# Kernel tuning notes

Hardware: AMD Instinct MI355X
Metric: run time of the kernel (lower is better)

Reference implementation:

```python
import jax, jax.numpy as jnp
import numpy as np

N = 50000      # nodes
E = 800000     # edges (before self-loops)
IN = 128       # in_channels
HID = 64       # hidden_channels (= per-head dim, concat=False)
H = 4          # heads
OUT = 40       # out_channels
L = 4          # num_layers
LN_EPS = 1e-5


def setup_inputs() -> dict:
    key = jax.random.key(0)
    ks = jax.random.split(key, 12)
    s = 0.05
    return {
        "x": jax.random.normal(ks[0], (N, IN), jnp.float32),
        "edge_index": jax.random.randint(ks[1], (2, E), 0, N, dtype=jnp.int32),
        "Wi": jax.random.normal(ks[2], (IN, HID), jnp.float32) * s,
        "bi": jnp.zeros((HID,), jnp.float32),
        "lin_W": jax.random.normal(ks[3], (L, HID, H * HID), jnp.float32) * s,
        "att_src": jax.random.normal(ks[4], (L, H, HID), jnp.float32) * s,
        "att_dst": jax.random.normal(ks[5], (L, H, HID), jnp.float32) * s,
        "gat_b": jnp.zeros((L, HID), jnp.float32),
        "ln_g": jnp.ones((L, HID), jnp.float32),
        "ln_b": jnp.zeros((L, HID), jnp.float32),
        "Wo": jax.random.normal(ks[6], (HID, OUT), jnp.float32) * s,
        "bo": jnp.zeros((OUT,), jnp.float32),
    }


def _layer_norm(x, g, b):
    mu = jnp.mean(x, axis=-1, keepdims=True)
    var = jnp.mean(jnp.square(x - mu), axis=-1, keepdims=True)
    return (x - mu) * jax.lax.rsqrt(var + LN_EPS) * g + b


def _gat_conv(x, src, dst, W, a_src, a_dst, bias):
    # PyG GATConv: heads=H, out_channels=HID, concat=False (mean over heads),
    # negative_slope=0.2, self-loops already appended to (src, dst).
    xl = (x @ W).reshape(N, H, HID)                    # [N,H,C]
    alpha_s = jnp.einsum('nhc,hc->nh', xl, a_src)      # [N,H]
    alpha_d = jnp.einsum('nhc,hc->nh', xl, a_dst)      # [N,H]
    e = jax.nn.leaky_relu(alpha_s[src] + alpha_d[dst], 0.2)  # [Etot,H]
    # segment softmax over incoming edges of each destination node
    m = jax.ops.segment_max(e, dst, num_segments=N)    # [N,H]
    e = jnp.exp(e - m[dst])
    denom = jax.ops.segment_sum(e, dst, num_segments=N)
    alpha = e / (denom[dst] + 1e-16)                   # [Etot,H]
    msg = alpha[:, :, None] * xl[src]                  # [Etot,H,C]
    out = jax.ops.segment_sum(msg, dst, num_segments=N)  # [N,H,C]
    return out.mean(axis=1) + bias                     # concat=False -> mean


def reference(x, edge_index, Wi, bi, lin_W, att_src, att_dst, gat_b, ln_g, ln_b, Wo, bo):
    # add self-loops (GATConv default add_self_loops=True)
    loops = jnp.arange(N, dtype=edge_index.dtype)
    src = jnp.concatenate([edge_index[0], loops])
    dst = jnp.concatenate([edge_index[1], loops])

    h = jax.nn.elu(x @ Wi + bi)
    for i in range(L):
        residual = h
        h = _gat_conv(h, src, dst, lin_W[i], att_src[i], att_dst[i], gat_b[i])
        h = _layer_norm(h, ln_g[i], ln_b[i])
        h = jax.nn.elu(h)
        if i > 0:
            h = h + residual
        # dropout p=0.0 -> identity
    return h @ Wo + bo
```

## Files before the change

kernel.cpp:

```cpp
#include <hip/hip_runtime.h>
#include <hip/hip_bf16.h>

#define N_NODES 50000
#define N_EDGES 800000
#define E_TOT   (N_EDGES + N_NODES)
#define IN_CH   128
#define HID     64
#define HEADS   4
#define OUT_CH  40
#define LAYERS  4
#define LN_EPS  1e-5f

#define AG_STRIDE  262
#define WC_STRIDE  68

__device__ __forceinline__ unsigned short f2bf(float f) {
    unsigned u = __float_as_uint(f);
    unsigned r = (u + 0x7fffu + ((u >> 16) & 1u)) >> 16;
    return (unsigned short)r;
}
__device__ __forceinline__ float bf_lo(unsigned u) { return __uint_as_float(u << 16); }
__device__ __forceinline__ float bf_hi(unsigned u) { return __uint_as_float(u & 0xffff0000u); }
__device__ __forceinline__ float lrelu(float x) { return x > 0.f ? x : 0.2f * x; }

__device__ __forceinline__ unsigned fenc(float f) {
    unsigned u = __float_as_uint(f);
    return (u & 0x80000000u) ? ~u : (u | 0x80000000u);
}
__device__ __forceinline__ float fdec(unsigned k) {
    unsigned u = (k & 0x80000000u) ? (k & 0x7fffffffu) : ~k;
    return __uint_as_float(u);
}


__global__ void k_hist(const int* __restrict__ ei, int* __restrict__ cnt,
                       int* __restrict__ rank) {
    int e = blockIdx.x * blockDim.x + threadIdx.x;
    if (e >= E_TOT) return;
    int dst = (e < N_EDGES) ? ei[N_EDGES + e] : (e - N_EDGES);
    rank[e] = atomicAdd(&cnt[dst], 1);
}

__global__ __launch_bounds__(1024) void k_scan_a(const int* __restrict__ cnt,
                                                 int* __restrict__ row_ptr,
                                                 int* __restrict__ bsum) {
    __shared__ int wt[16];
    int tid = threadIdx.x, lane = tid & 63, w = tid >> 6;
    int i = blockIdx.x * 1024 + tid;
    int v = (i < N_NODES) ? cnt[i] : 0;
    int x = v;
    for (int off = 1; off < 64; off <<= 1) {
        int t = __shfl_up(x, off, 64);
        if (lane >= off) x += t;
    }
    if (lane == 63) wt[w] = x;
    __syncthreads();
    if (w == 0) {
        int t = (lane < 16) ? wt[lane] : 0;
        for (int off = 1; off < 16; off <<= 1) {
            int u = __shfl_up(t, off, 64);
            if (lane >= off) t += u;
        }
        if (lane < 16) wt[lane] = t;
    }
    __syncthreads();
    int woff = (w > 0) ? wt[w - 1] : 0;
    if (i < N_NODES) row_ptr[i] = woff + x - v;
    if (tid == 0) bsum[blockIdx.x] = wt[15];
}

#define SCAN_BLOCKS 49

__global__ __launch_bounds__(64) void k_scan_b(const int* __restrict__ bsum,
                                               int* __restrict__ boff,
                                               int* __restrict__ row_ptr) {
    int lane = threadIdx.x;
    int v = (lane < SCAN_BLOCKS) ? bsum[lane] : 0;
    int x = v;
    for (int off = 1; off < 64; off <<= 1) {
        int t = __shfl_up(x, off, 64);
        if (lane >= off) x += t;
    }
    if (lane < SCAN_BLOCKS) boff[lane] = x - v;
    if (lane == 63) row_ptr[N_NODES] = x;
}

__global__ __launch_bounds__(256) void k_scan_c(int* __restrict__ row_ptr,
                                                const int* __restrict__ boff) {
    int i = blockIdx.x * 256 + threadIdx.x;
    if (i >= N_NODES) return;
    row_ptr[i] += boff[i >> 10];
}

__global__ void k_scatter(const int* __restrict__ ei,
                          const int* __restrict__ row_ptr,
                          const int* __restrict__ rank,
                          int* __restrict__ csr_src) {
    int e = blockIdx.x * blockDim.x + threadIdx.x;
    if (e >= E_TOT) return;
    int src, dst;
    if (e < N_EDGES) { src = ei[e]; dst = ei[N_EDGES + e]; }
    else             { src = dst = e - N_EDGES; }
    int pos = row_ptr[dst] + rank[e];
    csr_src[pos] = src;
}


__global__ __launch_bounds__(256) void k_prep(const float* __restrict__ lin_W,
                                              const float* __restrict__ att_src,
                                              const float* __restrict__ att_dst,
                                              float* __restrict__ watt,
                                              float* __restrict__ wstack) {
    int l = blockIdx.x, tid = threadIdx.x;
    const float* Wl = lin_W + (size_t)l * HID * 256;
    {
        int k = tid, h = k >> 6, i = k & 63;
        const float* src = Wl + i * 256 + h * 64;
        float* dstp = wstack + (size_t)l * 256 * 64 + k * 64;
        for (int c = 0; c < 64; c += 4)
            *(float4*)(dstp + c) = *(const float4*)(src + c);
    }
    for (int idx = tid; idx < 512; idx += 256) {
        int v = idx >> 6, i = idx & 63;
        int h = v & 3;
        const float* av = (v < 4 ? att_src : att_dst) + (size_t)l * 256 + h * 64;
        const float* wr = Wl + i * 256 + h * 64;
        float p = 0.f;
        for (int c = 0; c < 64; ++c) p = fmaf(wr[c], av[c], p);
        watt[(size_t)l * 512 + v * 64 + i] = p;
    }
}


__global__ __launch_bounds__(256) void k_gemm_in(const float* __restrict__ x,
                                                 const float* __restrict__ Wi,
                                                 const float* __restrict__ bi,
                                                 const float* __restrict__ watt,
                                                 float* __restrict__ h,
                                                 unsigned short* __restrict__ h_bf,
                                                 float* __restrict__ alpha_s,
                                                 float* __restrict__ alpha_d,
                                                 unsigned* __restrict__ mxk) {
    __shared__ float xT[IN_CH * 64];
    __shared__ float Ws[IN_CH * HID];
    __shared__ float wl[512];
    __shared__ unsigned s_mx[4];
    int tid = threadIdx.x;
    int row0 = blockIdx.x * 64;
    if (tid < 4) s_mx[tid] = 0;
    for (int i = tid; i < 512; i += 256) wl[i] = watt[i];
    for (int i = tid * 4; i < IN_CH * HID; i += 1024)
        *(float4*)(Ws + i) = *(const float4*)(Wi + i);
    {
        int r = tid >> 2, k0 = (tid & 3) * 32;
        int rr = row0 + r;
#pragma unroll
        for (int j = 0; j < 32; j += 4) {
            float4 v = (rr < N_NODES) ? *(const float4*)(x + (size_t)rr * IN_CH + k0 + j)
                                      : make_float4(0.f, 0.f, 0.f, 0.f);
            xT[(k0 + j    ) * 64 + r] = v.x;
            xT[(k0 + j + 1) * 64 + r] = v.y;
            xT[(k0 + j + 2) * 64 + r] = v.z;
            xT[(k0 + j + 3) * 64 + r] = v.w;
        }
    }
    __syncthreads();
    int tx = tid & 15, ty = tid >> 4;
    int c0 = tx * 4, r0 = ty * 4;
    float acc[4][4] = {};
    for (int k = 0; k < IN_CH; ++k) {
        float4 xv = *(const float4*)(xT + k * 64 + r0);
        float4 wv = *(const float4*)(Ws + k * HID + c0);
        float xr[4] = {xv.x, xv.y, xv.z, xv.w};
        float wc[4] = {wv.x, wv.y, wv.z, wv.w};
#pragma unroll
        for (int r = 0; r < 4; ++r)
#pragma unroll
            for (int c = 0; c < 4; ++c)
                acc[r][c] = fmaf(xr[r], wc[c], acc[r][c]);
    }
    float4 bv = *(const float4*)(bi + c0);
    float bcs[4] = {bv.x, bv.y, bv.z, bv.w};
    float rpmax[4] = {-1e30f, -1e30f, -1e30f, -1e30f};
#pragma unroll
    for (int r = 0; r < 4; ++r) {
        int rr = row0 + r0 + r;
        float vv[4];
#pragma unroll
        for (int c = 0; c < 4; ++c) {
            float t = acc[r][c] + bcs[c];
            vv[c] = t > 0.f ? t : (__expf(t) - 1.f);
        }
        if (rr < N_NODES) {
            *(float4*)(h + (size_t)rr * HID + c0) = make_float4(vv[0], vv[1], vv[2], vv[3]);
            unsigned short t4[4] = {f2bf(vv[0]), f2bf(vv[1]), f2bf(vv[2]), f2bf(vv[3])};
            *(uint2*)(h_bf + (size_t)rr * HID + c0) = *(uint2*)t4;
        }
        float red[8];
#pragma unroll
        for (int v = 0; v < 8; ++v) {
            const float* wv = wl + v * 64 + c0;
            float p = vv[0]*wv[0] + vv[1]*wv[1] + vv[2]*wv[2] + vv[3]*wv[3];
            p += __shfl_xor(p, 1, 64);
            p += __shfl_xor(p, 2, 64);
            p += __shfl_xor(p, 4, 64);
            p += __shfl_xor(p, 8, 64);
            red[v] = p;
        }
        if (tx == 0 && rr < N_NODES) {
            *(float4*)(alpha_s + (size_t)rr * 4) = make_float4(red[0], red[1], red[2], red[3]);
            *(float4*)(alpha_d + (size_t)rr * 4) = make_float4(red[4], red[5], red[6], red[7]);
#pragma unroll
            for (int hh = 0; hh < 4; ++hh) rpmax[hh] = fmaxf(rpmax[hh], red[hh]);
        }
    }
    if (tx == 0) {
#pragma unroll
        for (int hh = 0; hh < 4; ++hh) atomicMax(&s_mx[hh], fenc(rpmax[hh]));
    }
    __syncthreads();
    if (tid < 4) atomicMax(&mxk[tid], s_mx[tid]);
}


__global__ __launch_bounds__(256) void k_aggregate(
    const unsigned short* __restrict__ h_bf,
    const float* __restrict__ alpha_s,
    const float* __restrict__ alpha_d,
    const int* __restrict__ row_ptr,
    const int* __restrict__ csr_src,
    const unsigned* __restrict__ mxk,
    unsigned short* __restrict__ agg)
{
    int tid = threadIdx.x;
    int d = blockIdx.x * 32 + (tid >> 3);
    int q = tid & 7;
    if (d >= N_NODES) return;
    int start = row_ptr[d], end = row_ptr[d + 1];

    float4 ad = *(const float4*)(alpha_d + (size_t)d * 4);
    float mp0 = lrelu(fdec(mxk[0]) + ad.x);
    float mp1 = lrelu(fdec(mxk[1]) + ad.y);
    float mp2 = lrelu(fdec(mxk[2]) + ad.z);
    float mp3 = lrelu(fdec(mxk[3]) + ad.w);

    float acc[4][8] = {};
    float ds0 = 0.f, ds1 = 0.f, ds2 = 0.f, ds3 = 0.f;

    int s = csr_src[start];
    for (int e = start; e < end; ++e) {
        int sn = (e + 1 < end) ? csr_src[e + 1] : 0;
        float4 as = *(const float4*)(alpha_s + (size_t)s * 4);
        uint4 u = *(const uint4*)(h_bf + ((size_t)s << 6) + (q << 3));
        float w0 = __expf(lrelu(as.x + ad.x) - mp0);
        float w1 = __expf(lrelu(as.y + ad.y) - mp1);
        float w2 = __expf(lrelu(as.z + ad.z) - mp2);
        float w3 = __expf(lrelu(as.w + ad.w) - mp3);
        ds0 += w0; ds1 += w1; ds2 += w2; ds3 += w3;
        float f0 = bf_lo(u.x), f1 = bf_hi(u.x), f2 = bf_lo(u.y), f3 = bf_hi(u.y);
        float f4 = bf_lo(u.z), f5 = bf_hi(u.z), f6 = bf_lo(u.w), f7 = bf_hi(u.w);
        acc[0][0] = fmaf(w0, f0, acc[0][0]); acc[0][1] = fmaf(w0, f1, acc[0][1]);
        acc[0][2] = fmaf(w0, f2, acc[0][2]); acc[0][3] = fmaf(w0, f3, acc[0][3]);
        acc[0][4] = fmaf(w0, f4, acc[0][4]); acc[0][5] = fmaf(w0, f5, acc[0][5]);
        acc[0][6] = fmaf(w0, f6, acc[0][6]); acc[0][7] = fmaf(w0, f7, acc[0][7]);
        acc[1][0] = fmaf(w1, f0, acc[1][0]); acc[1][1] = fmaf(w1, f1, acc[1][1]);
        acc[1][2] = fmaf(w1, f2, acc[1][2]); acc[1][3] = fmaf(w1, f3, acc[1][3]);
        acc[1][4] = fmaf(w1, f4, acc[1][4]); acc[1][5] = fmaf(w1, f5, acc[1][5]);
        acc[1][6] = fmaf(w1, f6, acc[1][6]); acc[1][7] = fmaf(w1, f7, acc[1][7]);
        acc[2][0] = fmaf(w2, f0, acc[2][0]); acc[2][1] = fmaf(w2, f1, acc[2][1]);
        acc[2][2] = fmaf(w2, f2, acc[2][2]); acc[2][3] = fmaf(w2, f3, acc[2][3]);
        acc[2][4] = fmaf(w2, f4, acc[2][4]); acc[2][5] = fmaf(w2, f5, acc[2][5]);
        acc[2][6] = fmaf(w2, f6, acc[2][6]); acc[2][7] = fmaf(w2, f7, acc[2][7]);
        acc[3][0] = fmaf(w3, f0, acc[3][0]); acc[3][1] = fmaf(w3, f1, acc[3][1]);
        acc[3][2] = fmaf(w3, f2, acc[3][2]); acc[3][3] = fmaf(w3, f3, acc[3][3]);
        acc[3][4] = fmaf(w3, f4, acc[3][4]); acc[3][5] = fmaf(w3, f5, acc[3][5]);
        acc[3][6] = fmaf(w3, f6, acc[3][6]); acc[3][7] = fmaf(w3, f7, acc[3][7]);
        s = sn;
    }

    float inv[4] = {1.f / (ds0 + 1e-16f), 1.f / (ds1 + 1e-16f),
                    1.f / (ds2 + 1e-16f), 1.f / (ds3 + 1e-16f)};
    size_t base = (size_t)d * 256 + (q << 3);
#pragma unroll
    for (int hh = 0; hh < 4; ++hh) {
        unsigned short t8[8];
#pragma unroll
        for (int k = 0; k < 8; ++k) t8[k] = f2bf(acc[hh][k] * inv[hh]);
        *(uint4*)(agg + base + hh * 64) = *(uint4*)t8;
    }
}


__global__ __launch_bounds__(256) void k_post(const unsigned short* __restrict__ agg,
                                              const float* __restrict__ wstack,
                                              const float* __restrict__ gat_b,
                                              const float* __restrict__ ln_g,
                                              const float* __restrict__ ln_b,
                                              const float* __restrict__ h_res,
                                              const float* __restrict__ watt_next,
                                              float* __restrict__ h_out,
                                              unsigned short* __restrict__ hbf_out,
                                              float* __restrict__ alpha_s,
                                              float* __restrict__ alpha_d,
                                              unsigned* __restrict__ mxk_next,
                                              int use_res, int do_alpha) {
    __shared__ unsigned short aS[32 * AG_STRIDE];
    __shared__ float Wc[32 * WC_STRIDE];
    __shared__ unsigned s_mx[4];
    int tid = threadIdx.x;
    int row0 = blockIdx.x * 32;
    if (tid < 4) s_mx[tid] = 0;
    {
        int r = tid & 31, kc = (tid >> 5) * 32;
        int rr = row0 + r;
        unsigned short* dstp = aS + r * AG_STRIDE + kc;
        if (rr < N_NODES) {
            const unsigned short* src = agg + (size_t)rr * 256 + kc;
#pragma unroll
            for (int j = 0; j < 8; ++j)
                *(uint2*)(dstp + j * 4) = *(const uint2*)(src + j * 4);
        } else {
            uint2 z = make_uint2(0, 0);
#pragma unroll
            for (int j = 0; j < 8; ++j) *(uint2*)(dstp + j * 4) = z;
        }
    }

    int tx = tid & 15, ty = tid >> 4;
    int c0 = tx * 4, r0 = ty * 2;
    float acc[2][4] = {};

    int wk = tid >> 3;
    int wc8 = (tid & 7) * 8;
    for (int chunk = 0; chunk < 8; ++chunk) {
        __syncthreads();
        {
            const float* wsrc = wstack + (size_t)(chunk * 32 + wk) * 64 + wc8;
            float* wdst = Wc + wk * WC_STRIDE + wc8;
            *(float4*)(wdst)     = *(const float4*)(wsrc);
            *(float4*)(wdst + 4) = *(const float4*)(wsrc + 4);
        }
        __syncthreads();
        int kbase = chunk * 32;
#pragma unroll
        for (int kb = 0; kb < 8; ++kb) {
            int kl = kb * 4;
            float4 w0 = *(const float4*)(Wc + (kl + 0) * WC_STRIDE + c0);
            float4 w1 = *(const float4*)(Wc + (kl + 1) * WC_STRIDE + c0);
            float4 w2 = *(const float4*)(Wc + (kl + 2) * WC_STRIDE + c0);
            float4 w3 = *(const float4*)(Wc + (kl + 3) * WC_STRIDE + c0);
#pragma unroll
            for (int r = 0; r < 2; ++r) {
                uint2 au = *(const uint2*)(aS + (r0 + r) * AG_STRIDE + kbase + kl);
                float a0 = bf_lo(au.x), a1 = bf_hi(au.x), a2 = bf_lo(au.y), a3 = bf_hi(au.y);
                acc[r][0] = fmaf(a0, w0.x, fmaf(a1, w1.x, fmaf(a2, w2.x, fmaf(a3, w3.x, acc[r][0]))));
                acc[r][1] = fmaf(a0, w0.y, fmaf(a1, w1.y, fmaf(a2, w2.y, fmaf(a3, w3.y, acc[r][1]))));
                acc[r][2] = fmaf(a0, w0.z, fmaf(a1, w1.z, fmaf(a2, w2.z, fmaf(a3, w3.z, acc[r][2]))));
                acc[r][3] = fmaf(a0, w0.w, fmaf(a1, w1.w, fmaf(a2, w2.w, fmaf(a3, w3.w, acc[r][3]))));
            }
        }
    }

    float4 gb = *(const float4*)(gat_b + c0);
    float bias[4] = {gb.x, gb.y, gb.z, gb.w};
    float4 lg = *(const float4*)(ln_g + c0);
    float4 lb = *(const float4*)(ln_b + c0);
    float gg[4] = {lg.x, lg.y, lg.z, lg.w};
    float bb[4] = {lb.x, lb.y, lb.z, lb.w};
    float rpmax[4] = {-1e30f, -1e30f, -1e30f, -1e30f};
#pragma unroll
    for (int r = 0; r < 2; ++r) {
        int rr = row0 + r0 + r;
        float o[4];
#pragma unroll
        for (int c = 0; c < 4; ++c) o[c] = acc[r][c] * 0.25f + bias[c];
        float s = o[0] + o[1] + o[2] + o[3];
        float s2 = o[0]*o[0] + o[1]*o[1] + o[2]*o[2] + o[3]*o[3];
        for (int off = 1; off < 16; off <<= 1) {
            s  += __shfl_xor(s,  off, 64);
            s2 += __shfl_xor(s2, off, 64);
        }
        float mu = s * (1.f / 64.f);
        float var = s2 * (1.f / 64.f) - mu * mu;
        float rstd = rsqrtf(var + LN_EPS);
        float vv[4];
#pragma unroll
        for (int c = 0; c < 4; ++c) {
            float t = (o[c] - mu) * rstd * gg[c] + bb[c];
            vv[c] = t > 0.f ? t : (__expf(t) - 1.f);
        }
        if (rr < N_NODES) {
            if (use_res) {
                float4 rv = *(const float4*)(h_res + (size_t)rr * HID + c0);
                vv[0] += rv.x; vv[1] += rv.y; vv[2] += rv.z; vv[3] += rv.w;
            }
            *(float4*)(h_out + (size_t)rr * HID + c0) = make_float4(vv[0], vv[1], vv[2], vv[3]);
            unsigned short t4[4] = {f2bf(vv[0]), f2bf(vv[1]), f2bf(vv[2]), f2bf(vv[3])};
            *(uint2*)(hbf_out + (size_t)rr * HID + c0) = *(uint2*)t4;
        }
        if (do_alpha) {
            float red[8];
#pragma unroll
            for (int v = 0; v < 8; ++v) {
                const float* wv = watt_next + v * 64 + c0;
                float p = vv[0]*wv[0] + vv[1]*wv[1] + vv[2]*wv[2] + vv[3]*wv[3];
                p += __shfl_xor(p, 1, 64);
                p += __shfl_xor(p, 2, 64);
                p += __shfl_xor(p, 4, 64);
                p += __shfl_xor(p, 8, 64);
                red[v] = p;
            }
            if (tx == 0 && rr < N_NODES) {
                *(float4*)(alpha_s + (size_t)rr * 4) = make_float4(red[0], red[1], red[2], red[3]);
                *(float4*)(alpha_d + (size_t)rr * 4) = make_float4(red[4], red[5], red[6], red[7]);
#pragma unroll
                for (int hh = 0; hh < 4; ++hh) rpmax[hh] = fmaxf(rpmax[hh], red[hh]);
            }
        }
    }
    if (do_alpha) {
        if (tx == 0) {
#pragma unroll
            for (int hh = 0; hh < 4; ++hh) atomicMax(&s_mx[hh], fenc(rpmax[hh]));
        }
        __syncthreads();
        if (tid < 4) atomicMax(&mxk_next[tid], s_mx[tid]);
    }
}


__global__ __launch_bounds__(256) void k_gemm_out(const float* __restrict__ h,
                                                  const float* __restrict__ Wo,
                                                  const float* __restrict__ bo,
                                                  float* __restrict__ out) {
    __shared__ float Ws[HID * OUT_CH];
    __shared__ float hs[6 * HID];
    int tid = threadIdx.x;
    int row0 = blockIdx.x * 6;
    for (int i = tid; i < HID * OUT_CH; i += 256) Ws[i] = Wo[i];
    for (int i = tid; i < 6 * HID; i += 256) {
        int r = row0 + (i >> 6);
        hs[i] = (r < N_NODES) ? h[(size_t)r * HID + (i & 63)] : 0.f;
    }
    __syncthreads();
    if (tid < 240) {
        int r = tid / 40, o = tid - r * 40;
        int rr = row0 + r;
        if (rr < N_NODES) {
            float acc = bo[o];
            for (int k = 0; k < HID; ++k)
                acc = fmaf(hs[r * HID + k], Ws[k * OUT_CH + o], acc);
            out[(size_t)row0 * OUT_CH + tid] = acc;
        }
    }
}


extern "C" void kernel_launch(void* const* d_in, const int* in_sizes, int n_in,
                              void* d_out, int out_size, void* d_ws, size_t ws_size,
                              hipStream_t stream) {
    const float* x       = (const float*)d_in[0];
    const int*   ei      = (const int*)  d_in[1];
    const float* Wi      = (const float*)d_in[2];
    const float* bi      = (const float*)d_in[3];
    const float* lin_W   = (const float*)d_in[4];
    const float* att_src = (const float*)d_in[5];
    const float* att_dst = (const float*)d_in[6];
    const float* gat_b   = (const float*)d_in[7];
    const float* ln_g    = (const float*)d_in[8];
    const float* ln_b    = (const float*)d_in[9];
    const float* Wo      = (const float*)d_in[10];
    const float* bo      = (const float*)d_in[11];
    float* out = (float*)d_out;

    char* ws = (char*)d_ws;
    size_t off = 0;
    auto alloc = [&](size_t bytes) -> void* {
        void* p = ws + off;
        off += (bytes + 255) & ~(size_t)255;
        return p;
    };
    float*          h_a     = (float*)alloc((size_t)N_NODES * HID * 4);
    float*          h_b     = (float*)alloc((size_t)N_NODES * HID * 4);
    unsigned short* h_bf    = (unsigned short*)alloc((size_t)N_NODES * HID * 2);
    unsigned short* agg     = (unsigned short*)alloc((size_t)N_NODES * 256 * 2);
    float*          alpha_s = (float*)alloc((size_t)N_NODES * 4 * 4);
    float*          alpha_d = (float*)alloc((size_t)N_NODES * 4 * 4);
    int*            cnt     = (int*)  alloc((size_t)N_NODES * 4);
    int*            row_ptr = (int*)  alloc((size_t)(N_NODES + 1) * 4);
    int*            csr_src = (int*)  alloc((size_t)E_TOT * 4);
    int*            rank    = (int*)  alloc((size_t)E_TOT * 4);
    unsigned*       maxkey  = (unsigned*)alloc((size_t)LAYERS * 4 * 4);
    int*            bsum    = (int*)  alloc((size_t)SCAN_BLOCKS * 4);
    int*            boff    = (int*)  alloc((size_t)SCAN_BLOCKS * 4);
    float*          watt    = (float*)alloc((size_t)LAYERS * 8 * 64 * 4);
    float*          wstack  = (float*)alloc((size_t)LAYERS * 256 * 64 * 4);

    hipMemsetAsync(cnt, 0, (size_t)N_NODES * 4, stream);
    hipMemsetAsync(maxkey, 0, (size_t)LAYERS * 4 * 4, stream);

    int egrid = (E_TOT + 255) / 256;
    k_hist<<<egrid, 256, 0, stream>>>(ei, cnt, rank);
    k_scan_a<<<SCAN_BLOCKS, 1024, 0, stream>>>(cnt, row_ptr, bsum);
    k_scan_b<<<1, 64, 0, stream>>>(bsum, boff, row_ptr);
    k_scan_c<<<(N_NODES + 255) / 256, 256, 0, stream>>>(row_ptr, boff);
    k_scatter<<<egrid, 256, 0, stream>>>(ei, row_ptr, rank, csr_src);

    k_prep<<<LAYERS, 256, 0, stream>>>(lin_W, att_src, att_dst, watt, wstack);

    int rtiles = (N_NODES + 63) / 64;
    k_gemm_in<<<rtiles, 256, 0, stream>>>(x, Wi, bi, watt, h_a, h_bf,
                                          alpha_s, alpha_d, maxkey);

    float* h_cur = h_a;
    float* h_nxt = h_b;
    int aggrid = (N_NODES + 31) / 32;
    int pgrid  = (N_NODES + 31) / 32;
    for (int l = 0; l < LAYERS; ++l) {
        k_aggregate<<<aggrid, 256, 0, stream>>>(h_bf, alpha_s, alpha_d, row_ptr, csr_src,
                                                maxkey + l * 4, agg);
        int do_alpha = (l + 1 < LAYERS) ? 1 : 0;
        k_post<<<pgrid, 256, 0, stream>>>(agg, wstack + (size_t)l * 256 * 64,
                                          gat_b + (size_t)l * HID,
                                          ln_g + (size_t)l * HID,
                                          ln_b + (size_t)l * HID,
                                          h_cur,
                                          watt + (size_t)((l + 1) % LAYERS) * 512,
                                          h_nxt, h_bf,
                                          alpha_s, alpha_d,
                                          maxkey + (size_t)((l + 1) % LAYERS) * 4,
                                          l > 0 ? 1 : 0, do_alpha);
        float* t = h_cur; h_cur = h_nxt; h_nxt = t;
    }

    int ogrid = (N_NODES + 5) / 6;
    k_gemm_out<<<ogrid, 256, 0, stream>>>(h_cur, Wo, bo, out);
}
```

Baseline: 529.5 us.

## Fuse GAT aggregation with post-projection kernel and double-buffer node features

Merges the edge aggregation kernel and the per-layer projection/LayerNorm/ELU kernel into one, so aggregated results go straight into shared memory and no longer round-trip through a global 256-wide bf16 buffer. The bf16 features and attention logits become ping-pong buffers so one layer's writes cannot race with other blocks still gathering neighbour data. This removes one launch per layer and the agg write/read traffic. In exchange, the block's shared-memory footprint now spans the latency-bound gather phase, which may lower occupancy during the gather.

```diff
diff --git a/kernel.cpp b/kernel.cpp
--- a/kernel.cpp
+++ b/kernel.cpp
@@ -223,106 +223,92 @@
 }
 
 
-__global__ __launch_bounds__(256) void k_aggregate(
+__global__ __launch_bounds__(256) void k_layer(
     const unsigned short* __restrict__ h_bf,
     const float* __restrict__ alpha_s,
     const float* __restrict__ alpha_d,
     const int* __restrict__ row_ptr,
     const int* __restrict__ csr_src,
     const unsigned* __restrict__ mxk,
-    unsigned short* __restrict__ agg)
+    const float* __restrict__ wstack,
+    const float* __restrict__ gat_b,
+    const float* __restrict__ ln_g,
+    const float* __restrict__ ln_b,
+    const float* __restrict__ h_res,
+    const float* __restrict__ watt_next,
+    float* __restrict__ h_out,
+    unsigned short* __restrict__ hbf_out,
+    float* __restrict__ alpha_s_nxt,
+    float* __restrict__ alpha_d_nxt,
+    unsigned* __restrict__ mxk_next,
+    int use_res, int do_alpha)
 {
-    int tid = threadIdx.x;
-    int d = blockIdx.x * 32 + (tid >> 3);
-    int q = tid & 7;
-    if (d >= N_NODES) return;
-    int start = row_ptr[d], end = row_ptr[d + 1];
-
-    float4 ad = *(const float4*)(alpha_d + (size_t)d * 4);
-    float mp0 = lrelu(fdec(mxk[0]) + ad.x);
-    float mp1 = lrelu(fdec(mxk[1]) + ad.y);
-    float mp2 = lrelu(fdec(mxk[2]) + ad.z);
-    float mp3 = lrelu(fdec(mxk[3]) + ad.w);
-
-    float acc[4][8] = {};
-    float ds0 = 0.f, ds1 = 0.f, ds2 = 0.f, ds3 = 0.f;
-
-    int s = csr_src[start];
-    for (int e = start; e < end; ++e) {
-        int sn = (e + 1 < end) ? csr_src[e + 1] : 0;
-        float4 as = *(const float4*)(alpha_s + (size_t)s * 4);
-        uint4 u = *(const uint4*)(h_bf + ((size_t)s << 6) + (q << 3));
-        float w0 = __expf(lrelu(as.x + ad.x) - mp0);
-        float w1 = __expf(lrelu(as.y + ad.y) - mp1);
-        float w2 = __expf(lrelu(as.z + ad.z) - mp2);
-        float w3 = __expf(lrelu(as.w + ad.w) - mp3);
-        ds0 += w0; ds1 += w1; ds2 += w2; ds3 += w3;
-        float f0 = bf_lo(u.x), f1 = bf_hi(u.x), f2 = bf_lo(u.y), f3 = bf_hi(u.y);
-        float f4 = bf_lo(u.z), f5 = bf_hi(u.z), f6 = bf_lo(u.w), f7 = bf_hi(u.w);
-        acc[0][0] = fmaf(w0, f0, acc[0][0]); acc[0][1] = fmaf(w0, f1, acc[0][1]);
-        acc[0][2] = fmaf(w0, f2, acc[0][2]); acc[0][3] = fmaf(w0, f3, acc[0][3]);
-        acc[0][4] = fmaf(w0, f4, acc[0][4]); acc[0][5] = fmaf(w0, f5, acc[0][5]);
-        acc[0][6] = fmaf(w0, f6, acc[0][6]); acc[0][7] = fmaf(w0, f7, acc[0][7]);
-        acc[1][0] = fmaf(w1, f0, acc[1][0]); acc[1][1] = fmaf(w1, f1, acc[1][1]);
-        acc[1][2] = fmaf(w1, f2, acc[1][2]); acc[1][3] = fmaf(w1, f3, acc[1][3]);
-        acc[1][4] = fmaf(w1, f4, acc[1][4]); acc[1][5] = fmaf(w1, f5, acc[1][5]);
-        acc[1][6] = fmaf(w1, f6, acc[1][6]); acc[1][7] = fmaf(w1, f7, acc[1][7]);
-        acc[2][0] = fmaf(w2, f0, acc[2][0]); acc[2][1] = fmaf(w2, f1, acc[2][1]);
-        acc[2][2] = fmaf(w2, f2, acc[2][2]); acc[2][3] = fmaf(w2, f3, acc[2][3]);
-        acc[2][4] = fmaf(w2, f4, acc[2][4]); acc[2][5] = fmaf(w2, f5, acc[2][5]);
-        acc[2][6] = fmaf(w2, f6, acc[2][6]); acc[2][7] = fmaf(w2, f7, acc[2][7]);
-        acc[3][0] = fmaf(w3, f0, acc[3][0]); acc[3][1] = fmaf(w3, f1, acc[3][1]);
-        acc[3][2] = fmaf(w3, f2, acc[3][2]); acc[3][3] = fmaf(w3, f3, acc[3][3]);
-        acc[3][4] = fmaf(w3, f4, acc[3][4]); acc[3][5] = fmaf(w3, f5, acc[3][5]);
-        acc[3][6] = fmaf(w3, f6, acc[3][6]); acc[3][7] = fmaf(w3, f7, acc[3][7]);
-        s = sn;
-    }
-
-    float inv[4] = {1.f / (ds0 + 1e-16f), 1.f / (ds1 + 1e-16f),
-                    1.f / (ds2 + 1e-16f), 1.f / (ds3 + 1e-16f)};
-    size_t base = (size_t)d * 256 + (q << 3);
-#pragma unroll
-    for (int hh = 0; hh < 4; ++hh) {
-        unsigned short t8[8];
-#pragma unroll
-        for (int k = 0; k < 8; ++k) t8[k] = f2bf(acc[hh][k] * inv[hh]);
-        *(uint4*)(agg + base + hh * 64) = *(uint4*)t8;
-    }
-}
-
-
-__global__ __launch_bounds__(256) void k_post(const unsigned short* __restrict__ agg,
-                                              const float* __restrict__ wstack,
-                                              const float* __restrict__ gat_b,
-                                              const float* __restrict__ ln_g,
-                                              const float* __restrict__ ln_b,
-                                              const float* __restrict__ h_res,
-                                              const float* __restrict__ watt_next,
-                                              float* __restrict__ h_out,
-                                              unsigned short* __restrict__ hbf_out,
-                                              float* __restrict__ alpha_s,
-                                              float* __restrict__ alpha_d,
-                                              unsigned* __restrict__ mxk_next,
-                                              int use_res, int do_alpha) {
     __shared__ unsigned short aS[32 * AG_STRIDE];
     __shared__ float Wc[32 * WC_STRIDE];
     __shared__ unsigned s_mx[4];
     int tid = threadIdx.x;
     int row0 = blockIdx.x * 32;
     if (tid < 4) s_mx[tid] = 0;
+
     {
-        int r = tid & 31, kc = (tid >> 5) * 32;
-        int rr = row0 + r;
-        unsigned short* dstp = aS + r * AG_STRIDE + kc;
-        if (rr < N_NODES) {
-            const unsigned short* src = agg + (size_t)rr * 256 + kc;
-#pragma unroll
-            for (int j = 0; j < 8; ++j)
-                *(uint2*)(dstp + j * 4) = *(const uint2*)(src + j * 4);
+        int dl = tid >> 3, q = tid & 7;
+        int d = row0 + dl;
+        unsigned short* arow = aS + dl * AG_STRIDE + (q << 3);
+        if (d < N_NODES) {
+            int start = row_ptr[d], end = row_ptr[d + 1];
+            float4 ad = *(const float4*)(alpha_d + (size_t)d * 4);
+            float mp0 = lrelu(fdec(mxk[0]) + ad.x);
+            float mp1 = lrelu(fdec(mxk[1]) + ad.y);
+            float mp2 = lrelu(fdec(mxk[2]) + ad.z);
+            float mp3 = lrelu(fdec(mxk[3]) + ad.w);
+
+            float acc[4][8] = {};
+            float ds0 = 0.f, ds1 = 0.f, ds2 = 0.f, ds3 = 0.f;
+
+            int s = csr_src[start];
+            for (int e = start; e < end; ++e) {
+                int sn = (e + 1 < end) ? csr_src[e + 1] : 0;
+                float4 as = *(const float4*)(alpha_s + (size_t)s * 4);
+                uint4 u = *(const uint4*)(h_bf + ((size_t)s << 6) + (q << 3));
+                float w0 = __expf(lrelu(as.x + ad.x) - mp0);
+                float w1 = __expf(lrelu(as.y + ad.y) - mp1);
+                float w2 = __expf(lrelu(as.z + ad.z) - mp2);
+                float w3 = __expf(lrelu(as.w + ad.w) - mp3);
+                ds0 += w0; ds1 += w1; ds2 += w2; ds3 += w3;
+                float f0 = bf_lo(u.x), f1 = bf_hi(u.x), f2 = bf_lo(u.y), f3 = bf_hi(u.y);
+                float f4 = bf_lo(u.z), f5 = bf_hi(u.z), f6 = bf_lo(u.w), f7 = bf_hi(u.w);
+                acc[0][0] = fmaf(w0, f0, acc[0][0]); acc[0][1] = fmaf(w0, f1, acc[0][1]);
+                acc[0][2] = fmaf(w0, f2, acc[0][2]); acc[0][3] = fmaf(w0, f3, acc[0][3]);
+                acc[0][4] = fmaf(w0, f4, acc[0][4]); acc[0][5] = fmaf(w0, f5, acc[0][5]);
+                acc[0][6] = fmaf(w0, f6, acc[0][6]); acc[0][7] = fmaf(w0, f7, acc[0][7]);
+                acc[1][0] = fmaf(w1, f0, acc[1][0]); acc[1][1] = fmaf(w1, f1, acc[1][1]);
+                acc[1][2] = fmaf(w1, f2, acc[1][2]); acc[1][3] = fmaf(w1, f3, acc[1][3]);
+                acc[1][4] = fmaf(w1, f4, acc[1][4]); acc[1][5] = fmaf(w1, f5, acc[1][5]);
+                acc[1][6] = fmaf(w1, f6, acc[1][6]); acc[1][7] = fmaf(w1, f7, acc[1][7]);
+                acc[2][0] = fmaf(w2, f0, acc[2][0]); acc[2][1] = fmaf(w2, f1, acc[2][1]);
+                acc[2][2] = fmaf(w2, f2, acc[2][2]); acc[2][3] = fmaf(w2, f3, acc[2][3]);
+                acc[2][4] = fmaf(w2, f4, acc[2][4]); acc[2][5] = fmaf(w2, f5, acc[2][5]);
+                acc[2][6] = fmaf(w2, f6, acc[2][6]); acc[2][7] = fmaf(w2, f7, acc[2][7]);
+                acc[3][0] = fmaf(w3, f0, acc[3][0]); acc[3][1] = fmaf(w3, f1, acc[3][1]);
+                acc[3][2] = fmaf(w3, f2, acc[3][2]); acc[3][3] = fmaf(w3, f3, acc[3][3]);
+                acc[3][4] = fmaf(w3, f4, acc[3][4]); acc[3][5] = fmaf(w3, f5, acc[3][5]);
+                acc[3][6] = fmaf(w3, f6, acc[3][6]); acc[3][7] = fmaf(w3, f7, acc[3][7]);
+                s = sn;
+            }
+
+            float inv[4] = {1.f / (ds0 + 1e-16f), 1.f / (ds1 + 1e-16f),
+                            1.f / (ds2 + 1e-16f), 1.f / (ds3 + 1e-16f)};
+#pragma unroll
+            for (int hh = 0; hh < 4; ++hh) {
+                unsigned short t8[8];
+#pragma unroll
+                for (int k = 0; k < 8; ++k) t8[k] = f2bf(acc[hh][k] * inv[hh]);
+                *(uint4*)(arow + hh * 64) = *(uint4*)t8;
+            }
         } else {
-            uint2 z = make_uint2(0, 0);
-#pragma unroll
-            for (int j = 0; j < 8; ++j) *(uint2*)(dstp + j * 4) = z;
+            uint4 z = make_uint4(0, 0, 0, 0);
+#pragma unroll
+            for (int hh = 0; hh < 4; ++hh) *(uint4*)(arow + hh * 64) = z;
         }
     }
 
@@ -411,8 +397,8 @@
                 red[v] = p;
             }
             if (tx == 0 && rr < N_NODES) {
-                *(float4*)(alpha_s + (size_t)rr * 4) = make_float4(red[0], red[1], red[2], red[3]);
-                *(float4*)(alpha_d + (size_t)rr * 4) = make_float4(red[4], red[5], red[6], red[7]);
+                *(float4*)(alpha_s_nxt + (size_t)rr * 4) = make_float4(red[0], red[1], red[2], red[3]);
+                *(float4*)(alpha_d_nxt + (size_t)rr * 4) = make_float4(red[4], red[5], red[6], red[7]);
 #pragma unroll
                 for (int hh = 0; hh < 4; ++hh) rpmax[hh] = fmaxf(rpmax[hh], red[hh]);
             }
@@ -480,21 +466,23 @@
         off += (bytes + 255) & ~(size_t)255;
         return p;
     };
-    float*          h_a     = (float*)alloc((size_t)N_NODES * HID * 4);
-    float*          h_b     = (float*)alloc((size_t)N_NODES * HID * 4);
-    unsigned short* h_bf    = (unsigned short*)alloc((size_t)N_NODES * HID * 2);
-    unsigned short* agg     = (unsigned short*)alloc((size_t)N_NODES * 256 * 2);
-    float*          alpha_s = (float*)alloc((size_t)N_NODES * 4 * 4);
-    float*          alpha_d = (float*)alloc((size_t)N_NODES * 4 * 4);
-    int*            cnt     = (int*)  alloc((size_t)N_NODES * 4);
-    int*            row_ptr = (int*)  alloc((size_t)(N_NODES + 1) * 4);
-    int*            csr_src = (int*)  alloc((size_t)E_TOT * 4);
-    int*            rank    = (int*)  alloc((size_t)E_TOT * 4);
-    unsigned*       maxkey  = (unsigned*)alloc((size_t)LAYERS * 4 * 4);
-    int*            bsum    = (int*)  alloc((size_t)SCAN_BLOCKS * 4);
-    int*            boff    = (int*)  alloc((size_t)SCAN_BLOCKS * 4);
-    float*          watt    = (float*)alloc((size_t)LAYERS * 8 * 64 * 4);
-    float*          wstack  = (float*)alloc((size_t)LAYERS * 256 * 64 * 4);
+    float*          h_a      = (float*)alloc((size_t)N_NODES * HID * 4);
+    float*          h_b      = (float*)alloc((size_t)N_NODES * HID * 4);
+    unsigned short* hbf_a    = (unsigned short*)alloc((size_t)N_NODES * HID * 2);
+    unsigned short* hbf_b    = (unsigned short*)alloc((size_t)N_NODES * HID * 2);
+    float*          als_a    = (float*)alloc((size_t)N_NODES * 4 * 4);
+    float*          ald_a    = (float*)alloc((size_t)N_NODES * 4 * 4);
+    float*          als_b    = (float*)alloc((size_t)N_NODES * 4 * 4);
+    float*          ald_b    = (float*)alloc((size_t)N_NODES * 4 * 4);
+    int*            cnt      = (int*)  alloc((size_t)N_NODES * 4);
+    int*            row_ptr  = (int*)  alloc((size_t)(N_NODES + 1) * 4);
+    int*            csr_src  = (int*)  alloc((size_t)E_TOT * 4);
+    int*            rank     = (int*)  alloc((size_t)E_TOT * 4);
+    unsigned*       maxkey   = (unsigned*)alloc((size_t)LAYERS * 4 * 4);
+    int*            bsum     = (int*)  alloc((size_t)SCAN_BLOCKS * 4);
+    int*            boff     = (int*)  alloc((size_t)SCAN_BLOCKS * 4);
+    float*          watt     = (float*)alloc((size_t)LAYERS * 8 * 64 * 4);
+    float*          wstack   = (float*)alloc((size_t)LAYERS * 256 * 64 * 4);
 
     hipMemsetAsync(cnt, 0, (size_t)N_NODES * 4, stream);
     hipMemsetAsync(maxkey, 0, (size_t)LAYERS * 4 * 4, stream);
@@ -509,28 +497,32 @@
     k_prep<<<LAYERS, 256, 0, stream>>>(lin_W, att_src, att_dst, watt, wstack);
 
     int rtiles = (N_NODES + 63) / 64;
-    k_gemm_in<<<rtiles, 256, 0, stream>>>(x, Wi, bi, watt, h_a, h_bf,
-                                          alpha_s, alpha_d, maxkey);
-
-    float* h_cur = h_a;
-    float* h_nxt = h_b;
-    int aggrid = (N_NODES + 31) / 32;
-    int pgrid  = (N_NODES + 31) / 32;
+    k_gemm_in<<<rtiles, 256, 0, stream>>>(x, Wi, bi, watt, h_a, hbf_a,
+                                          als_a, ald_a, maxkey);
+
+    int lgrid = (N_NODES + 31) / 32;
+    float*          h_cur   = h_a;   float*          h_nxt   = h_b;
+    unsigned short* hbf_cur = hbf_a; unsigned short* hbf_nxt = hbf_b;
+    float* als_cur = als_a; float* ald_cur = ald_a;
+    float* als_nxt = als_b; float* ald_nxt = ald_b;
     for (int l = 0; l < LAYERS; ++l) {
-        k_aggregate<<<aggrid, 256, 0, stream>>>(h_bf, alpha_s, alpha_d, row_ptr, csr_src,
-                                                maxkey + l * 4, agg);
         int do_alpha = (l + 1 < LAYERS) ? 1 : 0;
-        k_post<<<pgrid, 256, 0, stream>>>(agg, wstack + (size_t)l * 256 * 64,
-                                          gat_b + (size_t)l * HID,
-                                          ln_g + (size_t)l * HID,
-                                          ln_b + (size_t)l * HID,
-                                          h_cur,
-                                          watt + (size_t)((l + 1) % LAYERS) * 512,
-                                          h_nxt, h_bf,
-                                          alpha_s, alpha_d,
-                                          maxkey + (size_t)((l + 1) % LAYERS) * 4,
-                                          l > 0 ? 1 : 0, do_alpha);
-        float* t = h_cur; h_cur = h_nxt; h_nxt = t;
+        k_layer<<<lgrid, 256, 0, stream>>>(hbf_cur, als_cur, ald_cur, row_ptr, csr_src,
+                                           maxkey + l * 4,
+                                           wstack + (size_t)l * 256 * 64,
+                                           gat_b + (size_t)l * HID,
+                                           ln_g + (size_t)l * HID,
+                                           ln_b + (size_t)l * HID,
+                                           h_cur,
+                                           watt + (size_t)((l + 1) % LAYERS) * 512,
+                                           h_nxt, hbf_nxt,
+                                           als_nxt, ald_nxt,
+                                           maxkey + (size_t)((l + 1) % LAYERS) * 4,
+                                           l > 0 ? 1 : 0, do_alpha);
+        { float* t = h_cur; h_cur = h_nxt; h_nxt = t; }
+        { unsigned short* t = hbf_cur; hbf_cur = hbf_nxt; hbf_nxt = t; }
+        { float* t = als_cur; als_cur = als_nxt; als_nxt = t; }
+        { float* t = ald_cur; ald_cur = ald_nxt; ald_nxt = t; }
     }
 
     int ogrid = (N_NODES + 5) / 6;
```

After: 499.9 us. 1.06x faster.
